# Kernel optimization log

Hardware: AMD Instinct MI355X
Metric: run time of the kernel (lower is better)

The kernel has to match this reference:

```python
import jax, jax.numpy as jnp
import numpy as np

VOCAB = 100000
SEQ = 2048
NSYN = 4
D = 300      # embedding_size
H1 = 300     # biLSTM output dim (150 per direction)
U = 150      # LSTM units per direction


def _lstm(x, Wk, Wr, b, reverse=False):
    """Keras-style LSTM over [S, D] -> [S, U]. Gate order i, f, g(cell), o."""
    if reverse:
        x = x[::-1]
    u = Wr.shape[0]

    def step(carry, xt):
        h, c = carry
        z = xt @ Wk + h @ Wr + b              # [4U]
        i, f, g, o = jnp.split(z, 4, axis=-1)
        i = jax.nn.sigmoid(i)
        f = jax.nn.sigmoid(f)
        g = jnp.tanh(g)
        o = jax.nn.sigmoid(o)
        c = f * c + i * g
        h = o * jnp.tanh(c)
        return (h, c), h

    init = (jnp.zeros((u,), x.dtype), jnp.zeros((u,), x.dtype))
    _, hs = jax.lax.scan(step, init, x)
    return hs[::-1] if reverse else hs


def setup_inputs() -> dict:
    key = jax.random.key(0)
    ks = jax.random.split(key, 14)
    w = 0.05  # small init so exp() attention coefficients stay stable
    return {
        "sentence": jax.random.randint(ks[0], (SEQ,), 0, VOCAB),
        "synonym_indices": jax.random.randint(ks[1], (VOCAB, NSYN), 0, VOCAB),
        "embedding_matrix": jax.random.normal(ks[2], (VOCAB, D), jnp.float32) * 0.1,
        # forward LSTM
        "Wk_f": jax.random.normal(ks[3], (D, 4 * U), jnp.float32) * w,
        "Wr_f": jax.random.normal(ks[4], (U, 4 * U), jnp.float32) * w,
        "b_f": jnp.zeros((4 * U,), jnp.float32),
        # backward LSTM
        "Wk_b": jax.random.normal(ks[5], (D, 4 * U), jnp.float32) * w,
        "Wr_b": jax.random.normal(ks[6], (U, 4 * U), jnp.float32) * w,
        "b_b": jnp.zeros((4 * U,), jnp.float32),
        # primary attention dense (h1 -> h1)
        "W1": jax.random.normal(ks[7], (H1, H1), jnp.float32) * w,
        "b1": jnp.zeros((H1,), jnp.float32),
        # secondary attention dense (h1 -> 1, tanh)
        "W2": jax.random.normal(ks[8], (H1, 1), jnp.float32) * w,
        "b2": jnp.zeros((1,), jnp.float32),
        # output heads
        "We": jax.random.normal(ks[9], (H1, 8), jnp.float32) * w,
        "be": jnp.zeros((8,), jnp.float32),
        "Ws": jax.random.normal(ks[10], (H1, 1), jnp.float32) * w,
        "bs": jnp.zeros((1,), jnp.float32),
    }


def reference(sentence, synonym_indices, embedding_matrix,
              Wk_f, Wr_f, b_f, Wk_b, Wr_b, b_b,
              W1, b1, W2, b2, We, be, Ws, bs):
    emb = embedding_matrix[sentence]                       # [S, D]
    hf = _lstm(emb, Wk_f, Wr_f, b_f)                       # [S, U]
    hb = _lstm(emb, Wk_b, Wr_b, b_b, reverse=True)         # [S, U]
    hidden = jnp.concatenate([hf, hb], axis=-1)            # [S, H1]

    # ---- primary attention (vectorized over all tokens) ----
    out = hidden @ W1 + b1                                 # [S, H1]
    S = sentence.shape[0]
    # Faithful off-by-one from the original loop: token 0 uses row 0,
    # token i (i>=1) uses out/hidden row i-1.
    idx = jnp.concatenate([jnp.zeros((1,), jnp.int32),
                           jnp.arange(S - 1, dtype=jnp.int32)])
    syn_emb = embedding_matrix[synonym_indices[sentence]]  # [S, NSYN, D]
    coeff = jnp.exp(jnp.einsum('skd,sd->sk', syn_emb, out[idx]))  # [S, NSYN]
    m = jnp.einsum('sk,skd->sd', coeff, syn_emb)           # [S, D]
    h_hats = m + hidden[idx]                               # [S, H1]

    # ---- secondary attention ----
    c2 = jnp.exp(jnp.tanh(h_hats @ W2 + b2))               # [S, 1]
    H = jnp.sum(c2 * h_hats, axis=0)[None, :]              # [1, H1]

    emotion_logits = H @ We + be                           # [1, 8]
    sentiment_logits = H @ Ws + bs                         # [1, 1]
    return (emotion_logits, sentiment_logits)
```

## Files before the change

### kernel.cpp

```cpp
#include <hip/hip_runtime.h>
#include <hip/hip_bf16.h>

#define SEQ   2048
#define DIM   300
#define UU    150
#define G4    600
#define H1    300
#define NSYN  4

typedef _Float16 half2v __attribute__((ext_vector_type(2)));
union HU { unsigned u; half2v h; };

static __device__ __forceinline__ float sigm(float x) { return 1.0f / (1.0f + __expf(-x)); }
static __device__ __forceinline__ float tanh_fast(float x) { return 1.0f - 2.0f / (1.0f + __expf(2.0f * x)); }

static __device__ __forceinline__ float dot2acc(unsigned w, int h, float acc) {
    asm("v_dot2_f32_f16 %0, %1, %2, %0" : "+v"(acc) : "v"(w), "s"(h));
    return acc;
}

#define LDS_BARRIER() asm volatile("s_waitcnt lgkmcnt(0)\n\ts_barrier" ::: "memory")

__global__ void xpre_kernel(const int* __restrict__ sentence,
                            const float* __restrict__ emb_mat,
                            const float* __restrict__ Wk_f,
                            const float* __restrict__ b_f,
                            const float* __restrict__ Wk_b,
                            const float* __restrict__ b_b,
                            float* __restrict__ Xf, float* __restrict__ Xb)
{
    const int dir = blockIdx.y;
    const float* Wk = dir ? Wk_b : Wk_f;
    const float* bb = dir ? b_b : b_f;
    float* X = dir ? Xb : Xf;

    const int s0  = blockIdx.x * 8;
    const int tid = threadIdx.x;

    __shared__ int   sids[8];
    __shared__ float embs[8][DIM];

    if (tid < 8) sids[tid] = sentence[s0 + tid];
    __syncthreads();
    for (int e = tid; e < 8 * DIM; e += 640) {
        int r = e / DIM, d = e - r * DIM;
        embs[r][d] = emb_mat[(long)sids[r] * DIM + d];
    }
    __syncthreads();

    if (tid < G4) {
        float acc[8];
        float bv = bb[tid];
        #pragma unroll
        for (int r = 0; r < 8; ++r) acc[r] = bv;
        for (int k = 0; k < DIM; ++k) {
            float wv = Wk[k * G4 + tid];
            #pragma unroll
            for (int r = 0; r < 8; ++r) acc[r] = fmaf(embs[r][k], wv, acc[r]);
        }
        #pragma unroll
        for (int r = 0; r < 8; ++r) X[(long)(s0 + r) * G4 + tid] = acc[r];
    }
}

#define REP75(F) \
  F(0) F(1) F(2) F(3) F(4) F(5) F(6) F(7) F(8) F(9) \
  F(10) F(11) F(12) F(13) F(14) F(15) F(16) F(17) F(18) F(19) \
  F(20) F(21) F(22) F(23) F(24) F(25) F(26) F(27) F(28) F(29) \
  F(30) F(31) F(32) F(33) F(34) F(35) F(36) F(37) F(38) F(39) \
  F(40) F(41) F(42) F(43) F(44) F(45) F(46) F(47) F(48) F(49) \
  F(50) F(51) F(52) F(53) F(54) F(55) F(56) F(57) F(58) F(59) \
  F(60) F(61) F(62) F(63) F(64) F(65) F(66) F(67) F(68) F(69) \
  F(70) F(71) F(72) F(73) F(74)

static __device__ __forceinline__ unsigned packpair(const float* __restrict__ Wr, int c, int k) {
    HU x;
    x.h.x = (_Float16)Wr[(2 * k) * G4 + c];
    x.h.y = (_Float16)Wr[(2 * k + 1) * G4 + c];
    return x.u;
}

__global__ __launch_bounds__(256) __attribute__((amdgpu_waves_per_eu(1, 1)))
void lstm_scan_kernel(
    const float* __restrict__ Xf, const float* __restrict__ Xb,
    const float* __restrict__ Wr_f, const float* __restrict__ Wr_b,
    float* __restrict__ hidden)
{
    const int dir = blockIdx.x;
    const float* X  = dir ? Xb : Xf;
    const float* Wr = dir ? Wr_b : Wr_f;
    const int tid  = threadIdx.x;
    const int lane = tid & 63;

    __shared__ float zs[G4];
    __shared__ __align__(4) _Float16 hs16[256];

    const int c0 = tid;
    const int c1 = tid + 256;
    const bool has2 = (tid < 88);
    const int c2 = has2 ? (tid + 512) : 599;

#define WDECL(k) unsigned wA_##k, wB_##k, wC_##k;
    REP75(WDECL)
#undef WDECL
#define WLOAD(k) wA_##k = packpair(Wr, c0, k); wB_##k = packpair(Wr, c1, k); wC_##k = packpair(Wr, c2, k);
    REP75(WLOAD)
#undef WLOAD

    if (tid < 128) ((unsigned*)hs16)[tid] = 0u;
    float c = 0.0f;

    int t = dir ? (SEQ - 1) : 0;
    const int dt = dir ? -1 : 1;
    float x0 = X[t * G4 + c0];
    float x1 = X[t * G4 + c1];
    float x2 = X[t * G4 + c2];
    __syncthreads();

    const unsigned* hp = (const unsigned*)hs16;

    for (int step = 0; step < SEQ; ++step) {
        const int tn = (step < SEQ - 1) ? (t + dt) : t;
        float xn0 = X[tn * G4 + c0];
        float xn1 = X[tn * G4 + c1];
        float xn2 = X[tn * G4 + c2];

        unsigned hr0 = hp[lane];
        unsigned hr1 = hp[64 + lane];

        float a0 = x0, a1 = x1, a2 = x2;
#define DOT(k) { int hk = ((k) < 64) ? __builtin_amdgcn_readlane((int)hr0, (k)) \
                                     : __builtin_amdgcn_readlane((int)hr1, (k) - 64); \
                 a0 = dot2acc(wA_##k, hk, a0); \
                 a1 = dot2acc(wB_##k, hk, a1); \
                 a2 = dot2acc(wC_##k, hk, a2); }
        REP75(DOT)
#undef DOT

        zs[c0] = a0;
        zs[c1] = a1;
        if (has2) zs[c2] = a2;
        LDS_BARRIER();

        if (tid < UU) {
            float zi = zs[tid], zf = zs[UU + tid], zg = zs[2 * UU + tid], zo = zs[3 * UU + tid];
            float ig = sigm(zi);
            float fg = sigm(zf);
            float gg = tanh_fast(zg);
            float og = sigm(zo);
            c = fg * c + ig * gg;
            float hv = og * tanh_fast(c);
            hs16[tid] = (_Float16)hv;
            hidden[(long)t * H1 + dir * UU + tid] = hv;
        }
        LDS_BARRIER();

        x0 = xn0; x1 = xn1; x2 = xn2;
        t = tn;
    }
}

__global__ void w1_kernel(const float* __restrict__ hidden,
                          const float* __restrict__ W1,
                          const float* __restrict__ b1,
                          float* __restrict__ outm)
{
    const int s0  = blockIdx.x * 8;
    const int tid = threadIdx.x;
    __shared__ float hl[8][H1];
    for (int e = tid; e < 8 * H1; e += 320)
        hl[e / H1][e - (e / H1) * H1] = hidden[(long)s0 * H1 + e];
    __syncthreads();

    if (tid < H1) {
        float acc[8];
        float bv = b1[tid];
        #pragma unroll
        for (int r = 0; r < 8; ++r) acc[r] = bv;
        for (int k = 0; k < H1; ++k) {
            float wv = W1[k * H1 + tid];
            #pragma unroll
            for (int r = 0; r < 8; ++r) acc[r] = fmaf(hl[r][k], wv, acc[r]);
        }
        #pragma unroll
        for (int r = 0; r < 8; ++r) outm[(long)(s0 + r) * H1 + tid] = acc[r];
    }
}

static __device__ __forceinline__ float4 blockReduce4(float4 v, float* red, int tid)
{
    #pragma unroll
    for (int off = 32; off > 0; off >>= 1) {
        v.x += __shfl_down(v.x, off);
        v.y += __shfl_down(v.y, off);
        v.z += __shfl_down(v.z, off);
        v.w += __shfl_down(v.w, off);
    }
    __syncthreads();
    if ((tid & 63) == 0) {
        int wv = tid >> 6;
        red[wv * 4 + 0] = v.x; red[wv * 4 + 1] = v.y;
        red[wv * 4 + 2] = v.z; red[wv * 4 + 3] = v.w;
    }
    __syncthreads();
    float4 r;
    r.x = red[0]; r.y = red[1]; r.z = red[2]; r.w = red[3];
    #pragma unroll
    for (int wv = 1; wv < 5; ++wv) {
        r.x += red[wv * 4 + 0]; r.y += red[wv * 4 + 1];
        r.z += red[wv * 4 + 2]; r.w += red[wv * 4 + 3];
    }
    return r;
}

static __device__ __forceinline__ float blockReduce1(float v, float* red, int tid)
{
    #pragma unroll
    for (int off = 32; off > 0; off >>= 1) v += __shfl_down(v, off);
    __syncthreads();
    if ((tid & 63) == 0) red[tid >> 6] = v;
    __syncthreads();
    return red[0] + red[1] + red[2] + red[3] + red[4];
}

__global__ void attn_kernel(const int* __restrict__ sentence,
                            const int* __restrict__ syn_idx,
                            const float* __restrict__ emb_mat,
                            const float* __restrict__ outm,
                            const float* __restrict__ hidden,
                            const float* __restrict__ W2,
                            const float* __restrict__ b2,
                            float* __restrict__ whh)
{
    const int s   = blockIdx.x;
    const int t   = s ? (s - 1) : 0;
    const int tid = threadIdx.x;
    __shared__ float red[20];

    const int sent = sentence[s];
    const long i0 = (long)syn_idx[sent * NSYN + 0] * DIM;
    const long i1 = (long)syn_idx[sent * NSYN + 1] * DIM;
    const long i2 = (long)syn_idx[sent * NSYN + 2] * DIM;
    const long i3 = (long)syn_idx[sent * NSYN + 3] * DIM;

    float se0 = 0.f, se1 = 0.f, se2 = 0.f, se3 = 0.f, od = 0.f, hd = 0.f;
    if (tid < DIM) {
        se0 = emb_mat[i0 + tid];
        se1 = emb_mat[i1 + tid];
        se2 = emb_mat[i2 + tid];
        se3 = emb_mat[i3 + tid];
        od  = outm[(long)t * H1 + tid];
        hd  = hidden[(long)t * H1 + tid];
    }

    float4 dots = blockReduce4(make_float4(se0 * od, se1 * od, se2 * od, se3 * od), red, tid);
    float c0 = __expf(dots.x), c1 = __expf(dots.y), c2c = __expf(dots.z), c3 = __expf(dots.w);

    float hh = fmaf(c0, se0, fmaf(c1, se1, fmaf(c2c, se2, fmaf(c3, se3, hd))));

    float w2v = (tid < DIM) ? W2[tid] : 0.f;
    float dot2 = blockReduce1(hh * w2v, red, tid);
    float cc = __expf(tanh_fast(dot2 + b2[0]));

    if (tid < DIM) whh[(long)s * H1 + tid] = cc * hh;
}

__global__ void hred_kernel(const float* __restrict__ whh, float* __restrict__ H)
{
    const int d   = blockIdx.x;
    const int tid = threadIdx.x;
    float acc = 0.f;
    for (int s = tid; s < SEQ; s += 256) acc += whh[(long)s * H1 + d];
    #pragma unroll
    for (int off = 32; off > 0; off >>= 1) acc += __shfl_down(acc, off);
    __shared__ float red[4];
    if ((tid & 63) == 0) red[tid >> 6] = acc;
    __syncthreads();
    if (tid == 0) H[d] = red[0] + red[1] + red[2] + red[3];
}

__global__ void logits_kernel(const float* __restrict__ H,
                              const float* __restrict__ We,
                              const float* __restrict__ be,
                              const float* __restrict__ Ws,
                              const float* __restrict__ bs,
                              float* __restrict__ outp)
{
    const int e = threadIdx.x;
    if (e < 9) {
        float acc = (e < 8) ? be[e] : bs[0];
        for (int d = 0; d < H1; ++d) {
            float wv = (e < 8) ? We[d * 8 + e] : Ws[d];
            acc = fmaf(H[d], wv, acc);
        }
        outp[e] = acc;
    }
}

extern "C" void kernel_launch(void* const* d_in, const int* in_sizes, int n_in,
                              void* d_out, int out_size, void* d_ws, size_t ws_size,
                              hipStream_t stream)
{
    const int* sentence   = (const int*)d_in[0];
    const int* syn_idx    = (const int*)d_in[1];
    const float* emb      = (const float*)d_in[2];
    const float* Wk_f     = (const float*)d_in[3];
    const float* Wr_f     = (const float*)d_in[4];
    const float* b_f      = (const float*)d_in[5];
    const float* Wk_b     = (const float*)d_in[6];
    const float* Wr_b     = (const float*)d_in[7];
    const float* b_b      = (const float*)d_in[8];
    const float* W1       = (const float*)d_in[9];
    const float* b1       = (const float*)d_in[10];
    const float* W2       = (const float*)d_in[11];
    const float* b2       = (const float*)d_in[12];
    const float* We       = (const float*)d_in[13];
    const float* be       = (const float*)d_in[14];
    const float* Ws       = (const float*)d_in[15];
    const float* bs       = (const float*)d_in[16];

    float* ws     = (float*)d_ws;
    float* Xf     = ws;
    float* Xb     = Xf + (long)SEQ * G4;
    float* hidden = Xb + (long)SEQ * G4;
    float* outm   = hidden + (long)SEQ * H1;
    float* whh    = outm + (long)SEQ * H1;
    float* H      = whh + (long)SEQ * H1;

    float* outp = (float*)d_out;

    xpre_kernel<<<dim3(SEQ / 8, 2), 640, 0, stream>>>(sentence, emb, Wk_f, b_f, Wk_b, b_b, Xf, Xb);
    lstm_scan_kernel<<<2, 256, 0, stream>>>(Xf, Xb, Wr_f, Wr_b, hidden);
    w1_kernel<<<SEQ / 8, 320, 0, stream>>>(hidden, W1, b1, outm);
    attn_kernel<<<SEQ, 320, 0, stream>>>(sentence, syn_idx, emb, outm, hidden, W2, b2, whh);
    hred_kernel<<<H1, 256, 0, stream>>>(whh, H);
    logits_kernel<<<1, 64, 0, stream>>>(H, We, be, Ws, bs, outp);
}
```

Measured before the change: 2.278 ms.

## Spread LSTM recurrence over 512 threads and split dot chains into even/odd accumulators

The recurrent scan kernel now launches 512 threads per direction, so each thread handles at most two gate columns instead of three. That roughly cuts the serial dot2 work per thread for each timestep. Each column's dot product is also split into two independent accumulator chains (even and odd k) to shorten the dependent latency chain. In exchange there are twice as many waves per block. Occupancy hints change to two waves per EU, which halves the register budget that has to hold the preloaded weights, and barrier cost may grow with more waves.

```diff
diff --git a/kernel.cpp b/kernel.cpp
--- a/kernel.cpp
+++ b/kernel.cpp
@@ -80,7 +80,7 @@
     return x.u;
 }
 
-__global__ __launch_bounds__(256) __attribute__((amdgpu_waves_per_eu(1, 1)))
+__global__ __launch_bounds__(512) __attribute__((amdgpu_waves_per_eu(2, 2)))
 void lstm_scan_kernel(
     const float* __restrict__ Xf, const float* __restrict__ Xb,
     const float* __restrict__ Wr_f, const float* __restrict__ Wr_b,
@@ -96,14 +96,13 @@
     __shared__ __align__(4) _Float16 hs16[256];
 
     const int c0 = tid;
-    const int c1 = tid + 256;
     const bool has2 = (tid < 88);
-    const int c2 = has2 ? (tid + 512) : 599;
-
-#define WDECL(k) unsigned wA_##k, wB_##k, wC_##k;
+    const int c1 = has2 ? (tid + 512) : 599;
+
+#define WDECL(k) unsigned wA_##k, wB_##k;
     REP75(WDECL)
 #undef WDECL
-#define WLOAD(k) wA_##k = packpair(Wr, c0, k); wB_##k = packpair(Wr, c1, k); wC_##k = packpair(Wr, c2, k);
+#define WLOAD(k) wA_##k = packpair(Wr, c0, k); wB_##k = packpair(Wr, c1, k);
     REP75(WLOAD)
 #undef WLOAD
 
@@ -114,7 +113,6 @@
     const int dt = dir ? -1 : 1;
     float x0 = X[t * G4 + c0];
     float x1 = X[t * G4 + c1];
-    float x2 = X[t * G4 + c2];
     __syncthreads();
 
     const unsigned* hp = (const unsigned*)hs16;
@@ -123,23 +121,36 @@
         const int tn = (step < SEQ - 1) ? (t + dt) : t;
         float xn0 = X[tn * G4 + c0];
         float xn1 = X[tn * G4 + c1];
-        float xn2 = X[tn * G4 + c2];
 
         unsigned hr0 = hp[lane];
         unsigned hr1 = hp[64 + lane];
 
-        float a0 = x0, a1 = x1, a2 = x2;
-#define DOT(k) { int hk = ((k) < 64) ? __builtin_amdgcn_readlane((int)hr0, (k)) \
-                                     : __builtin_amdgcn_readlane((int)hr1, (k) - 64); \
-                 a0 = dot2acc(wA_##k, hk, a0); \
-                 a1 = dot2acc(wB_##k, hk, a1); \
-                 a2 = dot2acc(wC_##k, hk, a2); }
-        REP75(DOT)
-#undef DOT
-
-        zs[c0] = a0;
-        zs[c1] = a1;
-        if (has2) zs[c2] = a2;
+        float a0e = x0, a0o = 0.0f, a1e = x1, a1o = 0.0f;
+#define RL(k) (((k) < 64) ? __builtin_amdgcn_readlane((int)hr0, (k)) \
+                          : __builtin_amdgcn_readlane((int)hr1, (k) - 64))
+#define DOTE(k) { int hk = RL(k); a0e = dot2acc(wA_##k, hk, a0e); a1e = dot2acc(wB_##k, hk, a1e); }
+#define DOTO(k) { int hk = RL(k); a0o = dot2acc(wA_##k, hk, a0o); a1o = dot2acc(wB_##k, hk, a1o); }
+        DOTE(0)  DOTO(1)  DOTE(2)  DOTO(3)  DOTE(4)
+        DOTO(5)  DOTE(6)  DOTO(7)  DOTE(8)  DOTO(9)
+        DOTE(10) DOTO(11) DOTE(12) DOTO(13) DOTE(14)
+        DOTO(15) DOTE(16) DOTO(17) DOTE(18) DOTO(19)
+        DOTE(20) DOTO(21) DOTE(22) DOTO(23) DOTE(24)
+        DOTO(25) DOTE(26) DOTO(27) DOTE(28) DOTO(29)
+        DOTE(30) DOTO(31) DOTE(32) DOTO(33) DOTE(34)
+        DOTO(35) DOTE(36) DOTO(37) DOTE(38) DOTO(39)
+        DOTE(40) DOTO(41) DOTE(42) DOTO(43) DOTE(44)
+        DOTO(45) DOTE(46) DOTO(47) DOTE(48) DOTO(49)
+        DOTE(50) DOTO(51) DOTE(52) DOTO(53) DOTE(54)
+        DOTO(55) DOTE(56) DOTO(57) DOTE(58) DOTO(59)
+        DOTE(60) DOTO(61) DOTE(62) DOTO(63) DOTE(64)
+        DOTO(65) DOTE(66) DOTO(67) DOTE(68) DOTO(69)
+        DOTE(70) DOTO(71) DOTE(72) DOTO(73) DOTE(74)
+#undef DOTE
+#undef DOTO
+#undef RL
+
+        zs[c0] = a0e + a0o;
+        if (has2) zs[c1] = a1e + a1o;
         LDS_BARRIER();
 
         if (tid < UU) {
@@ -155,7 +166,7 @@
         }
         LDS_BARRIER();
 
-        x0 = xn0; x1 = xn1; x2 = xn2;
+        x0 = xn0; x1 = xn1;
         t = tn;
     }
 }
@@ -330,7 +341,7 @@
     float* outp = (float*)d_out;
 
     xpre_kernel<<<dim3(SEQ / 8, 2), 640, 0, stream>>>(sentence, emb, Wk_f, b_f, Wk_b, b_b, Xf, Xb);
-    lstm_scan_kernel<<<2, 256, 0, stream>>>(Xf, Xb, Wr_f, Wr_b, hidden);
+    lstm_scan_kernel<<<2, 512, 0, stream>>>(Xf, Xb, Wr_f, Wr_b, hidden);
     w1_kernel<<<SEQ / 8, 320, 0, stream>>>(hidden, W1, b1, outm);
     attn_kernel<<<SEQ, 320, 0, stream>>>(sentence, syn_idx, emb, outm, hidden, W2, b2, whh);
     hred_kernel<<<H1, 256, 0, stream>>>(whh, H);
```

Result: slower. 2.871 ms (+26.1%).
